# Optimization experiments

Measured on AMD Instinct MI355X. Metric: run time of the kernel, lower is better.

The kernel has to match this reference:

```python
import jax, jax.numpy as jnp
import numpy as np
import math

B, CIN, CH, H, W = 4, 64, 32, 64, 64
M_CH, DEPTH, K = 4, 3, 8
NPF = CIN // 2  # num_pos_feats per axis; pos channels = 2*NPF = CIN
TEMPERATURE = 10000.0


def sine_pos(h, w, npf, temperature=TEMPERATURE):
    # PositionEmbeddingSine with normalize=False; cumsum of ones == arange(1, n+1)
    y_embed = jnp.arange(1, h + 1, dtype=jnp.float32)
    x_embed = jnp.arange(1, w + 1, dtype=jnp.float32)
    dim_t = jnp.arange(npf, dtype=jnp.float32)
    dim_t = temperature ** (2.0 * jnp.floor(dim_t / 2.0) / npf)
    pos_x = jnp.broadcast_to(x_embed[None, :, None] / dim_t, (h, w, npf))
    pos_y = jnp.broadcast_to(y_embed[:, None, None] / dim_t, (h, w, npf))

    def interleave(p):
        return jnp.stack([jnp.sin(p[..., 0::2]), jnp.cos(p[..., 1::2])], axis=-1).reshape(h, w, npf)

    pos = jnp.concatenate([interleave(pos_y), interleave(pos_x)], axis=-1)  # (h,w,2*npf)
    return jnp.transpose(pos, (2, 0, 1))  # (2*npf, h, w)


def conv2d(x, wgt, bias, pad):
    y = jax.lax.conv_general_dilated(
        x, wgt, window_strides=(1, 1), padding=[(pad, pad), (pad, pad)],
        dimension_numbers=('NCHW', 'OIHW', 'NCHW'))
    return y + bias[None, :, None, None]


def setup_inputs() -> dict:
    key = jax.random.key(0)
    ks = jax.random.split(key, 13)
    s = 0.05
    return {
        'f':    jax.random.normal(ks[0], (B, CH, H, W), jnp.float32),
        'map':  jax.random.normal(ks[1], (B, 1, 32, 32), jnp.float32),
        'f_q':  jax.random.normal(ks[2], (B, CIN, H, W), jnp.float32),
        'f_k':  jax.random.normal(ks[3], (B, CIN, H, W), jnp.float32),
        'm_k':  jax.random.normal(ks[4], (B, 1, 32, 32), jnp.float32),
        'wq':   jax.random.normal(ks[5], (M_CH, CIN), jnp.float32) * s,
        'wk':   jax.random.normal(ks[6], (M_CH, CIN), jnp.float32) * s,
        'w_in':  jax.random.normal(ks[7], (CH, CH, 1, 1), jnp.float32) * s,
        'b_in':  jax.random.normal(ks[8], (CH,), jnp.float32) * s,
        'w_mid': jax.random.normal(ks[9], (DEPTH, CH, CH, 3, 3), jnp.float32) * s,
        'b_mid': jax.random.normal(ks[10], (DEPTH, CH), jnp.float32) * s,
        'w_out': jax.random.normal(ks[11], (1, CH, 3, 3), jnp.float32) * s,
        'b_out': jax.random.normal(ks[12], (1,), jnp.float32) * s,
    }


def reference(f, map, f_q, f_k, m_k, wq, wk, w_in, b_in, w_mid, b_mid, w_out, b_out):
    b, c, h, w = f_q.shape
    hf, wf = f.shape[2], f.shape[3]
    # self.ret: bilinear resize to f's spatial size (align_corners=False)
    map_r = jax.image.resize(map, (b, 1, hf, wf), method='bilinear')
    m_k_r = jax.image.resize(m_k, (b, 1, hf, wf), method='bilinear')

    pos = sine_pos(h, w, NPF)[None]  # (1, CIN, h, w); same for pos_emb_h/pos_emb_l
    fq_emb = f_q + pos
    fk_emb = f_k + pos

    # 1x1 convs == channel matmuls
    query = jnp.einsum('mc,bchw->bhwm', wq, fq_emb).reshape(b, h * w, M_CH)  # (b, N, m)
    key_t = jnp.einsum('mc,bchw->bmhw', wk, fk_emb).reshape(b, M_CH, h * w)  # (b, m, N)

    sim = jnp.einsum('bqm,bmk->bqk', query, key_t)   # (b, N, N)
    sim = jax.nn.softmax(sim, axis=-2)                # softmax over query axis (dim=-2)

    value = (jnp.exp(m_k_r) / math.e).reshape(b, 1, h * w)  # broadcast over query axis
    context = sim * value
    context_k, _ = jax.lax.top_k(context, K)          # (b, N, K) over last (key) axis
    context_m = jnp.mean(context_k, axis=-1)          # (b, N)
    corrected_map = context_m.reshape(b, 1, h, w)

    corrected_map = corrected_map * map_r + map_r
    rmap = 1.0 - jax.nn.sigmoid(corrected_map)

    x = rmap * f  # broadcast over channel dim
    x = conv2d(x, w_in, b_in, 0)
    for i in range(DEPTH):
        x = jax.nn.relu(conv2d(x, w_mid[i], b_mid[i], 1))
    out = conv2d(x, w_out, b_out, 1) + corrected_map
    return (x, out, corrected_map)
```

## Files before the change

kernel.cpp:

```cpp
#include <hip/hip_runtime.h>
#include <hip/hip_bf16.h>
#include <math.h>

#define BB 4
#define CIN 64
#define CH 32
#define HH 64
#define WW 64
#define NN 4096
#define MCH 4
#define NQCH 32
#define LOG2E 1.4426950408889634f

#define PP_OFF     0
#define Q4_OFF     1024
#define K4_OFF     66560
#define CV_OFF     132096
#define CPSUM_OFF  672768
#define RMAP_OFF   148480
#define CMAPF_OFF  164864
#define T8_OFF     181248
#define XA_OFF     181248
#define XB_OFF     705536

#define OUT_X_OFF   0
#define OUT_O_OFF   524288
#define OUT_CM_OFF  540672

__device__ __forceinline__ float bilin32(const float* src, int b, int y, int x) {
    float sy = 0.5f * y - 0.25f;
    float sx = 0.5f * x - 0.25f;
    float fy0 = floorf(sy), fx0 = floorf(sx);
    int y0 = (int)fy0, x0 = (int)fx0;
    float fy = sy - fy0, fx = sx - fx0;
    int y0c = min(max(y0, 0), 31), y1c = min(max(y0 + 1, 0), 31);
    int x0c = min(max(x0, 0), 31), x1c = min(max(x0 + 1, 0), 31);
    const float* p = src + b * 1024;
    float v00 = p[y0c * 32 + x0c], v01 = p[y0c * 32 + x1c];
    float v10 = p[y1c * 32 + x0c], v11 = p[y1c * 32 + x1c];
    float v0 = v00 + fx * (v01 - v00);
    float v1 = v10 + fx * (v11 - v10);
    return v0 + fy * (v1 - v0);
}

__global__ void k0_posproj(const float* __restrict__ wq, const float* __restrict__ wk,
                           float* __restrict__ pp) {
    int t = threadIdx.x;
    float coord = (float)(t + 1);
    float qy[4] = {0,0,0,0}, qx[4] = {0,0,0,0}, ky[4] = {0,0,0,0}, kx[4] = {0,0,0,0};
    for (int c = 0; c < 32; ++c) {
        float e = (2.0f * (float)(c / 2)) / 32.0f;
        float dim = powf(10000.0f, e);
        float ang = coord / dim;
        float pr = (c & 1) ? cosf(ang) : sinf(ang);
        #pragma unroll
        for (int m = 0; m < 4; ++m) {
            qy[m] += wq[m * 64 + c] * pr;
            qx[m] += wq[m * 64 + 32 + c] * pr;
            ky[m] += wk[m * 64 + c] * pr;
            kx[m] += wk[m * 64 + 32 + c] * pr;
        }
    }
    #pragma unroll
    for (int m = 0; m < 4; ++m) {
        pp[0 * 256 + m * 64 + t] = qy[m];
        pp[1 * 256 + m * 64 + t] = qx[m];
        pp[2 * 256 + m * 64 + t] = ky[m];
        pp[3 * 256 + m * 64 + t] = kx[m];
    }
}

__global__ void k1_qk(const float* __restrict__ fq, const float* __restrict__ fk,
                      const float* __restrict__ wq, const float* __restrict__ wk,
                      const float* __restrict__ pp,
                      float* __restrict__ Q4, float* __restrict__ K4) {
    __shared__ float wqs[256], wks[256];
    __shared__ float red[256][9];
    int tid = threadIdx.x;
    wqs[tid] = wq[tid];
    wks[tid] = wk[tid];
    __syncthreads();
    int qi = tid & 63, g = tid >> 6;
    int gid = blockIdx.x * 64 + qi;
    int b = gid >> 12, hw = gid & 4095;
    const float* fqb = fq + (size_t)b * CIN * NN + hw;
    const float* fkb = fk + (size_t)b * CIN * NN + hw;
    float aq[4] = {0,0,0,0}, ak[4] = {0,0,0,0};
    int c0 = g * 16;
    #pragma unroll 4
    for (int c = c0; c < c0 + 16; ++c) {
        float vq = fqb[c * NN];
        float vk = fkb[c * NN];
        #pragma unroll
        for (int m = 0; m < 4; ++m) {
            aq[m] += wqs[m * 64 + c] * vq;
            ak[m] += wks[m * 64 + c] * vk;
        }
    }
    #pragma unroll
    for (int m = 0; m < 4; ++m) { red[tid][m] = aq[m]; red[tid][4 + m] = ak[m]; }
    __syncthreads();
    if (tid < 64) {
        int y = hw >> 6, x = hw & 63;
        float q4[4], k4[4];
        #pragma unroll
        for (int m = 0; m < 4; ++m) {
            q4[m] = LOG2E * (red[tid][m] + red[tid + 64][m] + red[tid + 128][m] + red[tid + 192][m]
                  + pp[0 * 256 + m * 64 + y] + pp[1 * 256 + m * 64 + x]);
            k4[m] = red[tid][4 + m] + red[tid + 64][4 + m] + red[tid + 128][4 + m] + red[tid + 192][4 + m]
                  + pp[2 * 256 + m * 64 + y] + pp[3 * 256 + m * 64 + x];
        }
        ((float4*)Q4)[gid] = make_float4(q4[0], q4[1], q4[2], q4[3]);
        ((float4*)K4)[gid] = make_float4(k4[0], k4[1], k4[2], k4[3]);
    }
}

__global__ void k2a_colstats(const float* __restrict__ Q4, const float* __restrict__ K4,
                             float* __restrict__ cpsum) {
    __shared__ float4 Qs[128];
    int blk = blockIdx.x;
    int kblk = blk & 7;   blk >>= 3;
    int qch  = blk & 31;  blk >>= 5;
    int b    = blk;
    int tid = threadIdx.x;
    if (tid < 128)
        Qs[tid] = ((const float4*)Q4)[b * NN + qch * 128 + tid];
    __syncthreads();
    int k0 = kblk * 512 + tid;
    float4 kva = ((const float4*)K4)[b * NN + k0];
    float4 kvb = ((const float4*)K4)[b * NN + k0 + 256];
    float sa = 0.0f, sb = 0.0f;
    #pragma unroll 8
    for (int i = 0; i < 128; ++i) {
        float4 q = Qs[i];
        float da = fmaf(q.x, kva.x, fmaf(q.y, kva.y, fmaf(q.z, kva.z, q.w * kva.w)));
        float db = fmaf(q.x, kvb.x, fmaf(q.y, kvb.y, fmaf(q.z, kvb.z, q.w * kvb.w)));
        sa += exp2f(da);
        sb += exp2f(db);
    }
    cpsum[(b * NQCH + qch) * NN + k0] = sa;
    cpsum[(b * NQCH + qch) * NN + k0 + 256] = sb;
}

__global__ void k2b_cmerge(const float* __restrict__ cpsum,
                           const float* __restrict__ m_k, float* __restrict__ cvals) {
    int gid = blockIdx.x * 256 + threadIdx.x;
    int b = gid >> 12, k = gid & 4095;
    float S = 0.0f;
    #pragma unroll
    for (int j = 0; j < NQCH; ++j) S += cpsum[(b * NQCH + j) * NN + k];
    float mk = bilin32(m_k, b, k >> 6, k & 63);
    cvals[gid] = LOG2E * (mk - 1.0f) - log2f(S);
}

__global__ void k3a_scan(const float* __restrict__ Q4, const float* __restrict__ K4,
                         const float* __restrict__ cvals, float* __restrict__ t8) {
    __shared__ float4 kvs[512];
    __shared__ float  cvs[512];
    int blk = blockIdx.x;
    int kc = blk & 7;   blk >>= 3;
    int g2 = blk & 15;  blk >>= 4;
    int b  = blk;
    int tid = threadIdx.x;
    int wave = tid >> 6, lane = tid & 63;

    const float4* Kb = (const float4*)K4 + b * NN + kc * 512;
    const float* cb = cvals + b * NN + kc * 512;
    #pragma unroll
    for (int i = tid; i < 512; i += 256) {
        kvs[i] = Kb[i];
        cvs[i] = cb[i];
    }
    __syncthreads();

    int qrow = (g2 * 4 + wave) * 64 + lane;
    float4 qv = ((const float4*)Q4)[b * NN + qrow];
    float t0 = -1e30f, t1 = -1e30f, t2 = -1e30f, t3 = -1e30f;
    float t4 = -1e30f, t5 = -1e30f, t6 = -1e30f, t7 = -1e30f;
    #pragma unroll 4
    for (int i = 0; i < 512; ++i) {
        float4 kv = kvs[i];
        float s = fmaf(qv.x, kv.x, fmaf(qv.y, kv.y,
                  fmaf(qv.z, kv.z, fmaf(qv.w, kv.w, cvs[i]))));
        if (s > t0) {
            float a = fmaxf(t0, s);
            t0 = fminf(a, t1); a = fmaxf(a, t1);
            t1 = fminf(a, t2); a = fmaxf(a, t2);
            t2 = fminf(a, t3); a = fmaxf(a, t3);
            t3 = fminf(a, t4); a = fmaxf(a, t4);
            t4 = fminf(a, t5); a = fmaxf(a, t5);
            t5 = fminf(a, t6); a = fmaxf(a, t6);
            t6 = fminf(a, t7); t7 = fmaxf(a, t7);
        }
    }
    float* o = t8 + ((size_t)(b * NN + qrow)) * 64 + kc * 8;
    o[0] = t0; o[1] = t1; o[2] = t2; o[3] = t3;
    o[4] = t4; o[5] = t5; o[6] = t6; o[7] = t7;
}

__global__ void k3b_merge(const float* __restrict__ t8, const float* __restrict__ mapin,
                          float* __restrict__ rmap, float* __restrict__ cmapf,
                          float* __restrict__ outp) {
    int tid = threadIdx.x;
    int qid = blockIdx.x * 4 + (tid >> 6);
    int lane = tid & 63;
    float v = t8[(size_t)qid * 64 + lane];
    float sm = 0.0f;
    #pragma unroll
    for (int r = 0; r < 8; ++r) {
        float m = v;
        int ln = lane;
        #pragma unroll
        for (int off = 32; off >= 1; off >>= 1) {
            float om = __shfl_xor(m, off);
            int ol = __shfl_xor(ln, off);
            if (om > m || (om == m && ol < ln)) { m = om; ln = ol; }
        }
        sm += exp2f(m);
        if (lane == ln) v = -1e30f;
    }
    if (lane == 0) {
        float cmv = sm * 0.125f;
        int b = qid >> 12, hw = qid & 4095;
        float mr = bilin32(mapin, b, hw >> 6, hw & 63);
        float cm = cmv * mr + mr;
        float rm = 1.0f / (1.0f + __expf(cm));
        rmap[qid] = rm;
        cmapf[qid] = cm;
        outp[OUT_CM_OFF + qid] = cm;
    }
}

__global__ void k4_conv1(const float* __restrict__ f, const float* __restrict__ rmap,
                         const float* __restrict__ w_in, const float* __restrict__ b_in,
                         float* __restrict__ xout) {
    __shared__ float ws_[1024];
    __shared__ float bs[32];
    int tid = threadIdx.x;
    for (int i = tid; i < 1024; i += 256) ws_[i] = w_in[i];
    if (tid < 32) bs[tid] = b_in[tid];
    __syncthreads();
    int gid = blockIdx.x * 256 + tid;
    int hw = gid & 4095;
    int og = (gid >> 12) & 7;
    int b  = gid >> 15;
    float rm = rmap[b * NN + hw];
    float acc[4];
    #pragma unroll
    for (int j = 0; j < 4; ++j) acc[j] = bs[og * 4 + j];
    const float* fb = f + (size_t)b * CH * NN + hw;
    for (int i = 0; i < 32; ++i) {
        float v = fb[i * NN] * rm;
        #pragma unroll
        for (int j = 0; j < 4; ++j) acc[j] += ws_[(og * 4 + j) * 32 + i] * v;
    }
    float* xo = xout + (size_t)b * CH * NN + (og * 4) * NN + hw;
    #pragma unroll
    for (int j = 0; j < 4; ++j) xo[j * NN] = acc[j];
}

__global__ void k5_conv3(const float* __restrict__ xin, const float* __restrict__ w,
                         const float* __restrict__ bias, float* __restrict__ xout,
                         float* __restrict__ outx) {
    __shared__ float tile[32][324];
    __shared__ float wsm[1152];
    __shared__ float bsm[4];
    int blk = blockIdx.x;
    int og = blk & 7;  blk >>= 3;
    int tx = blk & 3;  blk >>= 2;
    int ty = blk & 3;  blk >>= 2;
    int b  = blk;
    int tid = threadIdx.x;
    for (int i = tid; i < 1152; i += 256) wsm[i] = w[og * 1152 + i];
    if (tid < 4) bsm[tid] = bias[og * 4 + tid];
    int y0 = ty * 16 - 1, x0 = tx * 16 - 1;
    for (int i = tid; i < 32 * 324; i += 256) {
        int c = i / 324, r = i % 324;
        int yy = r / 18, xx = r % 18;
        int gy = y0 + yy, gx = x0 + xx;
        float v = 0.0f;
        if (gy >= 0 && gy < 64 && gx >= 0 && gx < 64)
            v = xin[((size_t)b * CH + c) * NN + gy * 64 + gx];
        tile[c][r] = v;
    }
    __syncthreads();
    int py = tid >> 4, px = tid & 15;
    float acc[4];
    #pragma unroll
    for (int j = 0; j < 4; ++j) acc[j] = bsm[j];
    for (int i = 0; i < 32; ++i) {
        const float* tr = &tile[i][py * 18 + px];
        float v00 = tr[0],  v01 = tr[1],  v02 = tr[2];
        float v10 = tr[18], v11 = tr[19], v12 = tr[20];
        float v20 = tr[36], v21 = tr[37], v22 = tr[38];
        #pragma unroll
        for (int j = 0; j < 4; ++j) {
            const float* wj = &wsm[j * 288 + i * 9];
            acc[j] += v00 * wj[0] + v01 * wj[1] + v02 * wj[2]
                    + v10 * wj[3] + v11 * wj[4] + v12 * wj[5]
                    + v20 * wj[6] + v21 * wj[7] + v22 * wj[8];
        }
    }
    size_t base = (size_t)b * CH * NN + (size_t)(og * 4) * NN
                + (ty * 16 + py) * 64 + tx * 16 + px;
    #pragma unroll
    for (int j = 0; j < 4; ++j) {
        float r_ = fmaxf(acc[j], 0.0f);
        xout[base + j * NN] = r_;
        if (outx) outx[base + j * NN] = r_;
    }
}

__global__ void k6_convout(const float* __restrict__ xin, const float* __restrict__ w_out,
                           const float* __restrict__ b_out, const float* __restrict__ cmapf,
                           float* __restrict__ outp) {
    __shared__ float wsm[288];
    __shared__ float red[256];
    int tid = threadIdx.x;
    for (int i = tid; i < 288; i += 256) wsm[i] = w_out[i];
    int pxi = tid & 63, g = tid >> 6;
    int gid = blockIdx.x * 64 + pxi;
    int b = gid >> 12, hw = gid & 4095;
    int y = hw >> 6, x = hw & 63;
    __syncthreads();
    float acc = 0.0f;
    int c0 = g * 8;
    for (int i = c0; i < c0 + 8; ++i) {
        const float* xi = xin + ((size_t)b * CH + i) * NN;
        #pragma unroll
        for (int ky = 0; ky < 3; ++ky) {
            int gy = y + ky - 1;
            if (gy < 0 || gy > 63) continue;
            #pragma unroll
            for (int kx = 0; kx < 3; ++kx) {
                int gx = x + kx - 1;
                if (gx < 0 || gx > 63) continue;
                acc += xi[gy * 64 + gx] * wsm[i * 9 + ky * 3 + kx];
            }
        }
    }
    red[tid] = acc;
    __syncthreads();
    if (tid < 64) {
        float a = red[tid] + red[tid + 64] + red[tid + 128] + red[tid + 192]
                + b_out[0] + cmapf[gid];
        outp[OUT_O_OFF + gid] = a;
    }
}

extern "C" void kernel_launch(void* const* d_in, const int* in_sizes, int n_in,
                              void* d_out, int out_size, void* d_ws, size_t ws_size,
                              hipStream_t stream) {
    const float* f     = (const float*)d_in[0];
    const float* mapin = (const float*)d_in[1];
    const float* f_q   = (const float*)d_in[2];
    const float* f_k   = (const float*)d_in[3];
    const float* m_k   = (const float*)d_in[4];
    const float* wq    = (const float*)d_in[5];
    const float* wk    = (const float*)d_in[6];
    const float* w_in  = (const float*)d_in[7];
    const float* b_in  = (const float*)d_in[8];
    const float* w_mid = (const float*)d_in[9];
    const float* b_mid = (const float*)d_in[10];
    const float* w_out = (const float*)d_in[11];
    const float* b_out = (const float*)d_in[12];
    float* outp = (float*)d_out;
    float* ws = (float*)d_ws;

    float* PP    = ws + PP_OFF;
    float* Q4    = ws + Q4_OFF;
    float* K4    = ws + K4_OFF;
    float* CV    = ws + CV_OFF;
    float* CPSUM = ws + CPSUM_OFF;
    float* RMAP  = ws + RMAP_OFF;
    float* CMAPF = ws + CMAPF_OFF;
    float* T8    = ws + T8_OFF;
    float* XA    = ws + XA_OFF;
    float* XB    = ws + XB_OFF;

    k0_posproj<<<1, 64, 0, stream>>>(wq, wk, PP);
    k1_qk<<<256, 256, 0, stream>>>(f_q, f_k, wq, wk, PP, Q4, K4);
    k2a_colstats<<<BB * NQCH * 8, 256, 0, stream>>>(Q4, K4, CPSUM);
    k2b_cmerge<<<64, 256, 0, stream>>>(CPSUM, m_k, CV);
    k3a_scan<<<BB * 16 * 8, 256, 0, stream>>>(Q4, K4, CV, T8);
    k3b_merge<<<BB * NN / 4, 256, 0, stream>>>(T8, mapin, RMAP, CMAPF, outp);
    k4_conv1<<<512, 256, 0, stream>>>(f, RMAP, w_in, b_in, XA);
    k5_conv3<<<512, 256, 0, stream>>>(XA, w_mid + 0 * 9216, b_mid + 0 * 32, XB, (float*)0);
    k5_conv3<<<512, 256, 0, stream>>>(XB, w_mid + 1 * 9216, b_mid + 1 * 32, XA, (float*)0);
    k5_conv3<<<512, 256, 0, stream>>>(XA, w_mid + 2 * 9216, b_mid + 2 * 32, XB, outp + OUT_X_OFF);
    k6_convout<<<256, 256, 0, stream>>>(XB, w_out, b_out, CMAPF, outp);
}
```

Baseline: 235.5 us.

## Batch top-8 scan with sorting networks and read Q/K directly from global

```diff
diff --git a/kernel.cpp b/kernel.cpp
--- a/kernel.cpp
+++ b/kernel.cpp
@@ -26,6 +26,8 @@
 #define OUT_X_OFF   0
 #define OUT_O_OFF   524288
 #define OUT_CM_OFF  540672
+
+#define CE(x, y) { float ce_lo = fminf(x, y); y = fmaxf(x, y); x = ce_lo; }
 
 __device__ __forceinline__ float bilin32(const float* src, int b, int y, int x) {
     float sy = 0.5f * y - 0.25f;
@@ -70,15 +72,15 @@
     }
 }
 
-__global__ void k1_qk(const float* __restrict__ fq, const float* __restrict__ fk,
-                      const float* __restrict__ wq, const float* __restrict__ wk,
-                      const float* __restrict__ pp,
-                      float* __restrict__ Q4, float* __restrict__ K4) {
+__global__ __launch_bounds__(512) void k1_qk(
+        const float* __restrict__ fq, const float* __restrict__ fk,
+        const float* __restrict__ wq, const float* __restrict__ wk,
+        const float* __restrict__ pp,
+        float* __restrict__ Q4, float* __restrict__ K4) {
     __shared__ float wqs[256], wks[256];
-    __shared__ float red[256][9];
-    int tid = threadIdx.x;
-    wqs[tid] = wq[tid];
-    wks[tid] = wk[tid];
+    __shared__ float red[512][9];
+    int tid = threadIdx.x;
+    if (tid < 256) { wqs[tid] = wq[tid]; wks[tid] = wk[tid]; }
     __syncthreads();
     int qi = tid & 63, g = tid >> 6;
     int gid = blockIdx.x * 64 + qi;
@@ -86,9 +88,9 @@
     const float* fqb = fq + (size_t)b * CIN * NN + hw;
     const float* fkb = fk + (size_t)b * CIN * NN + hw;
     float aq[4] = {0,0,0,0}, ak[4] = {0,0,0,0};
-    int c0 = g * 16;
-    #pragma unroll 4
-    for (int c = c0; c < c0 + 16; ++c) {
+    int c0 = g * 8;
+    #pragma unroll
+    for (int c = c0; c < c0 + 8; ++c) {
         float vq = fqb[c * NN];
         float vk = fkb[c * NN];
         #pragma unroll
@@ -105,10 +107,14 @@
         float q4[4], k4[4];
         #pragma unroll
         for (int m = 0; m < 4; ++m) {
-            q4[m] = LOG2E * (red[tid][m] + red[tid + 64][m] + red[tid + 128][m] + red[tid + 192][m]
-                  + pp[0 * 256 + m * 64 + y] + pp[1 * 256 + m * 64 + x]);
-            k4[m] = red[tid][4 + m] + red[tid + 64][4 + m] + red[tid + 128][4 + m] + red[tid + 192][4 + m]
-                  + pp[2 * 256 + m * 64 + y] + pp[3 * 256 + m * 64 + x];
+            float sq = 0.0f, sk = 0.0f;
+            #pragma unroll
+            for (int j = 0; j < 8; ++j) {
+                sq += red[tid + 64 * j][m];
+                sk += red[tid + 64 * j][4 + m];
+            }
+            q4[m] = LOG2E * (sq + pp[0 * 256 + m * 64 + y] + pp[1 * 256 + m * 64 + x]);
+            k4[m] = sk + pp[2 * 256 + m * 64 + y] + pp[3 * 256 + m * 64 + x];
         }
         ((float4*)Q4)[gid] = make_float4(q4[0], q4[1], q4[2], q4[3]);
         ((float4*)K4)[gid] = make_float4(k4[0], k4[1], k4[2], k4[3]);
@@ -117,22 +123,19 @@
 
 __global__ void k2a_colstats(const float* __restrict__ Q4, const float* __restrict__ K4,
                              float* __restrict__ cpsum) {
-    __shared__ float4 Qs[128];
     int blk = blockIdx.x;
     int kblk = blk & 7;   blk >>= 3;
     int qch  = blk & 31;  blk >>= 5;
     int b    = blk;
     int tid = threadIdx.x;
-    if (tid < 128)
-        Qs[tid] = ((const float4*)Q4)[b * NN + qch * 128 + tid];
-    __syncthreads();
+    const float4* Qg = (const float4*)Q4 + b * NN + qch * 128;
     int k0 = kblk * 512 + tid;
     float4 kva = ((const float4*)K4)[b * NN + k0];
     float4 kvb = ((const float4*)K4)[b * NN + k0 + 256];
     float sa = 0.0f, sb = 0.0f;
     #pragma unroll 8
     for (int i = 0; i < 128; ++i) {
-        float4 q = Qs[i];
+        float4 q = Qg[i];
         float da = fmaf(q.x, kva.x, fmaf(q.y, kva.y, fmaf(q.z, kva.z, q.w * kva.w)));
         float db = fmaf(q.x, kvb.x, fmaf(q.y, kvb.y, fmaf(q.z, kvb.z, q.w * kvb.w)));
         sa += exp2f(da);
@@ -153,44 +156,51 @@
     cvals[gid] = LOG2E * (mk - 1.0f) - log2f(S);
 }
 
-__global__ void k3a_scan(const float* __restrict__ Q4, const float* __restrict__ K4,
-                         const float* __restrict__ cvals, float* __restrict__ t8) {
-    __shared__ float4 kvs[512];
-    __shared__ float  cvs[512];
+__global__ __launch_bounds__(256) void k3a_scan(
+        const float* __restrict__ Q4, const float* __restrict__ K4,
+        const float* __restrict__ cvals, float* __restrict__ t8) {
     int blk = blockIdx.x;
     int kc = blk & 7;   blk >>= 3;
-    int g2 = blk & 15;  blk >>= 4;
+    int g4 = blk & 15;  blk >>= 4;
     int b  = blk;
     int tid = threadIdx.x;
     int wave = tid >> 6, lane = tid & 63;
-
+    int qrow = (g4 * 4 + wave) * 64 + lane;
+    float4 qv = ((const float4*)Q4)[b * NN + qrow];
     const float4* Kb = (const float4*)K4 + b * NN + kc * 512;
     const float* cb = cvals + b * NN + kc * 512;
-    #pragma unroll
-    for (int i = tid; i < 512; i += 256) {
-        kvs[i] = Kb[i];
-        cvs[i] = cb[i];
-    }
-    __syncthreads();
-
-    int qrow = (g2 * 4 + wave) * 64 + lane;
-    float4 qv = ((const float4*)Q4)[b * NN + qrow];
-    float t0 = -1e30f, t1 = -1e30f, t2 = -1e30f, t3 = -1e30f;
-    float t4 = -1e30f, t5 = -1e30f, t6 = -1e30f, t7 = -1e30f;
-    #pragma unroll 4
-    for (int i = 0; i < 512; ++i) {
-        float4 kv = kvs[i];
-        float s = fmaf(qv.x, kv.x, fmaf(qv.y, kv.y,
-                  fmaf(qv.z, kv.z, fmaf(qv.w, kv.w, cvs[i]))));
-        if (s > t0) {
-            float a = fmaxf(t0, s);
-            t0 = fminf(a, t1); a = fmaxf(a, t1);
-            t1 = fminf(a, t2); a = fmaxf(a, t2);
-            t2 = fminf(a, t3); a = fmaxf(a, t3);
-            t3 = fminf(a, t4); a = fmaxf(a, t4);
-            t4 = fminf(a, t5); a = fmaxf(a, t5);
-            t5 = fminf(a, t6); a = fmaxf(a, t6);
-            t6 = fminf(a, t7); t7 = fmaxf(a, t7);
+
+    float t0=-1e30f,t1=-1e30f,t2=-1e30f,t3=-1e30f;
+    float t4=-1e30f,t5=-1e30f,t6=-1e30f,t7=-1e30f;
+
+    #pragma unroll 2
+    for (int i0 = 0; i0 < 512; i0 += 8) {
+        float4 k0 = Kb[i0 + 0]; float4 k1 = Kb[i0 + 1];
+        float4 k2 = Kb[i0 + 2]; float4 k3 = Kb[i0 + 3];
+        float4 k4 = Kb[i0 + 4]; float4 k5 = Kb[i0 + 5];
+        float4 k6 = Kb[i0 + 6]; float4 k7 = Kb[i0 + 7];
+        float s0 = fmaf(qv.x,k0.x, fmaf(qv.y,k0.y, fmaf(qv.z,k0.z, qv.w*k0.w))) + cb[i0+0];
+        float s1 = fmaf(qv.x,k1.x, fmaf(qv.y,k1.y, fmaf(qv.z,k1.z, qv.w*k1.w))) + cb[i0+1];
+        float s2 = fmaf(qv.x,k2.x, fmaf(qv.y,k2.y, fmaf(qv.z,k2.z, qv.w*k2.w))) + cb[i0+2];
+        float s3 = fmaf(qv.x,k3.x, fmaf(qv.y,k3.y, fmaf(qv.z,k3.z, qv.w*k3.w))) + cb[i0+3];
+        float s4 = fmaf(qv.x,k4.x, fmaf(qv.y,k4.y, fmaf(qv.z,k4.z, qv.w*k4.w))) + cb[i0+4];
+        float s5 = fmaf(qv.x,k5.x, fmaf(qv.y,k5.y, fmaf(qv.z,k5.z, qv.w*k5.w))) + cb[i0+5];
+        float s6 = fmaf(qv.x,k6.x, fmaf(qv.y,k6.y, fmaf(qv.z,k6.z, qv.w*k6.w))) + cb[i0+6];
+        float s7 = fmaf(qv.x,k7.x, fmaf(qv.y,k7.y, fmaf(qv.z,k7.z, qv.w*k7.w))) + cb[i0+7];
+        float bm = fmaxf(fmaxf(fmaxf(s0,s1), fmaxf(s2,s3)),
+                         fmaxf(fmaxf(s4,s5), fmaxf(s6,s7)));
+        if (bm > t0) {
+            CE(s0,s1); CE(s2,s3); CE(s4,s5); CE(s6,s7);
+            CE(s0,s2); CE(s1,s3); CE(s4,s6); CE(s5,s7);
+            CE(s1,s2); CE(s5,s6);
+            CE(s0,s4); CE(s1,s5); CE(s2,s6); CE(s3,s7);
+            CE(s2,s4); CE(s3,s5);
+            CE(s1,s2); CE(s3,s4); CE(s5,s6);
+            t0 = fmaxf(t0, s7); t1 = fmaxf(t1, s6); t2 = fmaxf(t2, s5); t3 = fmaxf(t3, s4);
+            t4 = fmaxf(t4, s3); t5 = fmaxf(t5, s2); t6 = fmaxf(t6, s1); t7 = fmaxf(t7, s0);
+            CE(t0,t4); CE(t1,t5); CE(t2,t6); CE(t3,t7);
+            CE(t0,t2); CE(t1,t3); CE(t4,t6); CE(t5,t7);
+            CE(t0,t1); CE(t2,t3); CE(t4,t5); CE(t6,t7);
         }
     }
     float* o = t8 + ((size_t)(b * NN + qrow)) * 64 + kc * 8;
@@ -379,7 +389,7 @@
     float* XB    = ws + XB_OFF;
 
     k0_posproj<<<1, 64, 0, stream>>>(wq, wk, PP);
-    k1_qk<<<256, 256, 0, stream>>>(f_q, f_k, wq, wk, PP, Q4, K4);
+    k1_qk<<<256, 512, 0, stream>>>(f_q, f_k, wq, wk, PP, Q4, K4);
     k2a_colstats<<<BB * NQCH * 8, 256, 0, stream>>>(Q4, K4, CPSUM);
     k2b_cmerge<<<64, 256, 0, stream>>>(CPSUM, m_k, CV);
     k3a_scan<<<BB * 16 * 8, 256, 0, stream>>>(Q4, K4, CV, T8);
```

Result: faster. 223.5 us (-5.1%).
